# Kernel tuning notes

Measured on AMD Instinct MI355X. Metric: run time of the kernel, lower is better.

## Reference

```python
import jax, jax.numpy as jnp
import numpy as np

QNUM = 8
B, Q, K = 8, 32, 32
DIM = 2 ** QNUM  # v-circuit state dim; attn circuit uses 2*DIM (extra ancilla wire 0)

# --- 2x2 gate matrices (torchquantum conventions) ---

def ry_mat(theta):
    c = jnp.cos(theta / 2).astype(jnp.complex64)
    s = jnp.sin(theta / 2).astype(jnp.complex64)
    return jnp.stack([jnp.stack([c, -s], -1), jnp.stack([s, c], -1)], -2)

def rz_mat(theta):
    e = jnp.exp(-0.5j * theta)
    f = jnp.exp(0.5j * theta)
    z = jnp.zeros_like(e)
    return jnp.stack([jnp.stack([e, z], -1), jnp.stack([z, f], -1)], -2)

# --- state-vector gate application; wire 0 is the most-significant bit ---

def apply_1q(state, n, w, U):
    b = state.shape[0]
    st = state.reshape(b, 2 ** w, 2, 2 ** (n - w - 1))
    sub = 'bij,bajc->baic' if U.ndim == 3 else 'ij,bajc->baic'
    return jnp.einsum(sub, U, st).reshape(b, 2 ** n)

def apply_cnot(state, n, c, t):
    b = state.shape[0]
    st = state.reshape((b,) + (2,) * n)
    ca, ta = c + 1, t + 1
    c0 = jnp.take(st, 0, axis=ca)
    c1 = jnp.take(st, 1, axis=ca)
    c1 = jnp.flip(c1, axis=ta - 1 if ta > ca else ta)
    return jnp.stack([c0, c1], axis=ca).reshape(b, 2 ** n)

def apply_x(state, n, w):
    b = state.shape[0]
    st = state.reshape(b, 2 ** w, 2, -1)
    return jnp.flip(st, axis=2).reshape(b, 2 ** n)

def reset_wire(state, n, w):
    # torchquantum Reset: zero the |1> amplitude of the wire (no renorm)
    b = state.shape[0]
    st = state.reshape(b, 2 ** w, 2, -1)
    return st.at[:, :, 1, :].set(0).reshape(b, 2 ** n)

def init_state(b, n):
    return jnp.zeros((b, 2 ** n), jnp.complex64).at[:, 0].set(1)

# --- circuits ---

def v_circuit(value_flat, v_param):
    n = QNUM
    state = init_state(value_flat.shape[0], n)
    for i in range(n):  # v_embed: RY(value_i) on wire i (per-batch angle)
        state = apply_1q(state, n, i, ry_mat(value_flat[:, i]))
    for rep in range(6):  # inner_strent, repeat=6
        for i in range(n):  # fused RZ-RY-RZ (scalar params, shared over batch)
            U = rz_mat(v_param[rep, 2, i]) @ ry_mat(v_param[rep, 1, i]) @ rz_mat(v_param[rep, 0, i])
            state = apply_1q(state, n, i, U)
        for i in range(n):
            tg = (i + 1 + rep) % n
            if i == tg:
                tg = (tg + 1) % n
            state = apply_cnot(state, n, i, tg)
    return state

def attn_circuit(q_flat, k_flat, qk_param, attn_param):
    n = QNUM + 1  # wire 0 is the ancilla
    state = init_state(q_flat.shape[0], n)
    for i in range(QNUM):  # q_embed on wires 1..QNUM
        state = apply_1q(state, n, i + 1, ry_mat(q_flat[:, i]))
    for i in range(QNUM):  # RZ(qk[0,i]) then RY(qk[1,i]) fused
        state = apply_1q(state, n, i + 1, ry_mat(qk_param[1, i]) @ rz_mat(qk_param[0, i]))
    for i in range(QNUM):  # k_embed with -key
        state = apply_1q(state, n, i + 1, ry_mat(-k_flat[:, i]))
    state = apply_x(state, n, 0)
    for i in range(QNUM - 1):
        state = apply_1q(state, n, i + 1, ry_mat(attn_param[0, i]))
        state = apply_1q(state, n, i + 2, ry_mat(attn_param[1, i]))
        state = apply_cnot(state, n, i + 1, i + 2)
    state = apply_1q(state, n, QNUM, ry_mat(attn_param[0, QNUM - 1]))
    state = apply_1q(state, n, 0, ry_mat(attn_param[1, QNUM - 1]))
    state = apply_cnot(state, n, QNUM, 0)
    for w in range(1, QNUM + 1):
        state = reset_wire(state, n, w)
    return state

def forward(query, key, value, v_param, qk_param, attn_param):
    nb, nq, _ = query.shape
    nk = key.shape[1]
    # v circuit params/angles are independent of the query index, so simulate
    # over B*K and broadcast (identical math to the original B*Q*K repeat)
    v_states = v_circuit(value.reshape(nb * nk, QNUM), v_param).reshape(nb, nk, DIM)
    qf = jnp.broadcast_to(query[:, :, None, :], (nb, nq, nk, QNUM)).reshape(-1, QNUM)
    kf = jnp.broadcast_to(key[:, None, :, :], (nb, nq, nk, QNUM)).reshape(-1, QNUM)
    attn = attn_circuit(qf, kf, qk_param, attn_param).reshape(nb, nq, nk, 2, DIM)
    a0 = attn[:, :, :, 0, 0]  # amplitude of |00...0>
    a1 = attn[:, :, :, 1, 0]  # amplitude of |10...0> (ancilla=1)
    # sequential mixing v_new <- a0[k]*v_new + a1[k]*v_k, init e0; closed form:
    rev = jnp.flip(a0, axis=2)
    ecp = jnp.concatenate([jnp.ones_like(rev[:, :, :1]), jnp.cumprod(rev, axis=2)[:, :, :-1]], axis=2)
    suffix = jnp.flip(ecp, axis=2)  # suffix[j] = prod_{k>j} a0[k]
    total = jnp.prod(a0, axis=2)
    v_new = jnp.einsum('bqk,bkd->bqd', suffix * a1, v_states)
    v_new = v_new.at[:, :, 0].add(total)
    # StateEncoder normalization + MeasureAll(PauliZ)
    probs = v_new.real ** 2 + v_new.imag ** 2
    idx = jnp.arange(DIM)
    bits = (idx[None, :] >> (QNUM - 1 - jnp.arange(QNUM)[:, None])) & 1
    signs = (1 - 2 * bits).astype(jnp.float32)
    return jnp.einsum('bqd,wd->bqw', probs, signs) / jnp.sum(probs, -1, keepdims=True)

def setup_inputs():
    ks = jax.random.split(jax.random.key(0), 6)
    sigma = np.pi / 3
    return {
        'query': jax.random.normal(ks[0], (B, Q, QNUM), jnp.float32),
        'key': jax.random.normal(ks[1], (B, K, QNUM), jnp.float32),
        'value': jax.random.normal(ks[2], (B, K, QNUM), jnp.float32),
        'v_param': sigma * jax.random.normal(ks[3], (6, 3, QNUM), jnp.float32),
        'qk_param': sigma * jax.random.normal(ks[4], (3, QNUM), jnp.float32),
        'attn_param': sigma * jax.random.normal(ks[5], (2, QNUM), jnp.float32),
    }

def reference(query, key, value, v_param, qk_param, attn_param):
    return forward(query, key, value, v_param, qk_param, attn_param)
```

## Files before the change

### kernel.cpp

```cpp
#include <hip/hip_runtime.h>
#include <math.h>

#define NB 8
#define NQ 32
#define NK 32
#define DIM 256

struct c32 { float x, y; };
__device__ __forceinline__ c32 cmul(c32 a, c32 b) {
    return { a.x*b.x - a.y*b.y, a.x*b.y + a.y*b.x };
}

struct Maps { unsigned char m[6][8]; unsigned char r[6][8]; unsigned char fin[8]; };

constexpr unsigned gstep(int rep, unsigned y, int i) {
    int tgt = (i + 1 + rep) % 8;
    return y ^ (((y >> (7 - i)) & 1u) << (7 - tgt));
}
constexpr unsigned Lmap(int rep, unsigned x) {
    unsigned y = x;
    for (int i = 7; i >= 0; --i) y = gstep(rep, y, i);
    return y;
}
constexpr unsigned Linvmap(int rep, unsigned x) {
    unsigned y = x;
    for (int i = 0; i < 8; ++i) y = gstep(rep, y, i);
    return y;
}
constexpr Maps make_maps() {
    Maps mp{};
    unsigned Mc[8], Mic[8];
    for (int j2 = 0; j2 < 8; ++j2) { Mc[j2] = 1u << j2; Mic[j2] = 1u << j2; }
    for (int rep = 0; rep < 6; ++rep) {
        for (int bb = 0; bb < 8; ++bb) {
            mp.m[rep][bb] = (unsigned char)Mc[bb];
            unsigned row = 0;
            for (int k = 0; k < 8; ++k) row |= ((Mic[k] >> bb) & 1u) << k;
            mp.r[rep][bb] = (unsigned char)row;
        }
        unsigned nM[8], nMi[8];
        for (int j2 = 0; j2 < 8; ++j2) {
            unsigned v = Lmap(rep, 1u << j2), acc = 0;
            for (int k = 0; k < 8; ++k) if ((v >> k) & 1u) acc ^= Mc[k];
            nM[j2]  = acc;
            nMi[j2] = Linvmap(rep, Mic[j2]);
        }
        for (int j2 = 0; j2 < 8; ++j2) { Mc[j2] = nM[j2]; Mic[j2] = nMi[j2]; }
    }
    for (int j2 = 0; j2 < 8; ++j2) mp.fin[j2] = (unsigned char)Mic[j2];
    return mp;
}
constexpr Maps MAPS = make_maps();


__global__ __launch_bounds__(128) void k1_sim_coef(
        const float* __restrict__ query, const float* __restrict__ key,
        const float* __restrict__ value, const float* __restrict__ v_param,
        const float* __restrict__ qk_param, const float* __restrict__ attn_param,
        float2* __restrict__ vs, float2* __restrict__ coefg) {
    const int s  = blockIdx.x;
    const int b  = s >> 5;
    const int j  = s & 31;
    const int t  = threadIdx.x;
    const int ln = t & 63;

    if (t < 64) {
        __shared__ float2 U[48][4];
        if (ln < 48) {
            int rep = ln >> 3, w = ln & 7;
            float a   = v_param[(rep*3 + 0)*8 + w];
            float bb2 = v_param[(rep*3 + 1)*8 + w];
            float c   = v_param[(rep*3 + 2)*8 + w];
            float sb, cb;     __sincosf(bb2*0.5f, &sb, &cb);
            float sapc, capc; __sincosf((a + c)*0.5f, &sapc, &capc);
            float samc, camc; __sincosf((a - c)*0.5f, &samc, &camc);
            U[ln][0] = make_float2( cb*capc, -cb*sapc);
            U[ln][1] = make_float2(-sb*camc, -sb*samc);
            U[ln][2] = make_float2( sb*camc, -sb*samc);
            U[ln][3] = make_float2( cb*capc,  cb*sapc);
        }
        float cv[8], sv[8];
        #pragma unroll
        for (int i = 0; i < 8; ++i) __sincosf(value[s*8 + i]*0.5f, &sv[i], &cv[i]);
        float common = 1.f;
        #pragma unroll
        for (int i = 0; i < 6; ++i)
            common *= ((ln >> (5 - i)) & 1) ? sv[i] : cv[i];
        float2 amp[4];
        amp[0] = make_float2(common*cv[6]*cv[7], 0.f);
        amp[1] = make_float2(common*cv[6]*sv[7], 0.f);
        amp[2] = make_float2(common*sv[6]*cv[7], 0.f);
        amp[3] = make_float2(common*sv[6]*sv[7], 0.f);

        #pragma unroll
        for (int rep = 0; rep < 6; ++rep) {
            #pragma unroll
            for (int w = 0; w < 8; ++w) {
                const int g = rep*8 + w;
                const unsigned mm = MAPS.m[rep][7 - w];
                const unsigned rb = MAPS.r[rep][7 - w];
                const unsigned lm = mm >> 2;
                const unsigned sm = mm & 3;
                const float2 u00 = U[g][0], u01 = U[g][1];
                const float2 u10 = U[g][2], u11 = U[g][3];
                float2 P[4];
                if (sm == 0)      { P[0]=amp[0]; P[1]=amp[1]; P[2]=amp[2]; P[3]=amp[3]; }
                else if (sm == 1) { P[0]=amp[1]; P[1]=amp[0]; P[2]=amp[3]; P[3]=amp[2]; }
                else if (sm == 2) { P[0]=amp[2]; P[1]=amp[3]; P[2]=amp[0]; P[3]=amp[1]; }
                else              { P[0]=amp[3]; P[1]=amp[2]; P[2]=amp[1]; P[3]=amp[0]; }
                if (lm) {
                    #pragma unroll
                    for (int r2 = 0; r2 < 4; ++r2) {
                        P[r2].x = __shfl_xor(P[r2].x, (int)lm);
                        P[r2].y = __shfl_xor(P[r2].y, (int)lm);
                    }
                }
                const unsigned hx = __popc((unsigned)(ln << 2) & rb) & 1u;
                float2 na[4];
                #pragma unroll
                for (int r2 = 0; r2 < 4; ++r2) {
                    const bool h = (hx ^ (__popc((unsigned)r2 & rb) & 1u)) != 0u;
                    const float2 uo = h ? u11 : u00;
                    const float2 up = h ? u10 : u01;
                    na[r2].x = uo.x*amp[r2].x - uo.y*amp[r2].y + up.x*P[r2].x - up.y*P[r2].y;
                    na[r2].y = uo.x*amp[r2].y + uo.y*amp[r2].x + up.x*P[r2].y + up.y*P[r2].x;
                }
                #pragma unroll
                for (int r2 = 0; r2 < 4; ++r2) amp[r2] = na[r2];
            }
        }
        unsigned c0 = 0;
        #pragma unroll
        for (int kk = 0; kk < 6; ++kk)
            c0 ^= ((ln >> kk) & 1) ? (unsigned)MAPS.fin[kk + 2] : 0u;
        const int kst = j;
        float2* base = vs + ((size_t)(b*16 + (kst >> 1)) * 256) * 2 + (kst & 1);
        #pragma unroll
        for (int r2 = 0; r2 < 4; ++r2) {
            unsigned c = c0 ^ ((r2 & 1) ? (unsigned)MAPS.fin[0] : 0u)
                            ^ ((r2 & 2) ? (unsigned)MAPS.fin[1] : 0u);
            base[c*2] = amp[r2];
        }
    } else {
        const int k = ln >> 1, h = ln & 1;
        c32 f = { 1.f, 0.f };
        #pragma unroll
        for (int ii = 0; ii < 4; ++ii) {
            const int i = h*4 + ii;
            float qi  = query[(b*NQ + j)*8 + i];
            float ki  = key[(b*NK + k)*8 + i];
            float phi = attn_param[i] + ((i > 0) ? attn_param[8 + i - 1] : 0.f);
            float Th  = phi + qk_param[8 + i] - ki;
            float gam = qk_param[i] * 0.5f;
            c32 fi = {  __cosf(gam) * __cosf((Th + qi)*0.5f),
                       -__sinf(gam) * __cosf((Th - qi)*0.5f) };
            f = cmul(f, fi);
        }
        {
            c32 o2 = { __shfl_xor(f.x, 1), __shfl_xor(f.y, 1) };
            f = cmul(f, o2);
        }
        float fx = __shfl(f.x, 2*ln);
        float fy = __shfl(f.y, 2*ln);
        if (ln < 32) {
            const int kk = ln;
            float h7 = attn_param[15] * 0.5f;
            float s7 = __sinf(h7), c7 = __cosf(h7);
            c32 a0 = { -s7*fx, -s7*fy };
            c32 a1 = {  c7*fx,  c7*fy };
            c32 acc = a0;
            #pragma unroll
            for (int off = 1; off < 32; off <<= 1) {
                c32 v = { __shfl_down(acc.x, off), __shfl_down(acc.y, off) };
                if (kk + off < 32) acc = cmul(acc, v);
            }
            c32 S = { __shfl_down(acc.x, 1), __shfl_down(acc.y, 1) };
            if (kk == 31) { S.x = 1.f; S.y = 0.f; }
            c32 cf = cmul(S, a1);
            coefg[s*34 + kk] = make_float2(cf.x, cf.y);
            if (kk == 0) coefg[s*34 + 32] = make_float2(acc.x, acc.y);
        }
    }
}

__global__ __launch_bounds__(256) void k2_combine(
        const float2* __restrict__ vs, const float2* __restrict__ coefg,
        float* __restrict__ out) {
    const int bq = blockIdx.x;
    const int b = bq >> 5;
    const int q = bq & 31;
    const int t = threadIdx.x;

    __shared__ float2 coefL[33];
    __shared__ float prob[256];

    if (t < 33) coefL[t] = coefg[bq*34 + t];
    __syncthreads();

    {
        const float4* vb4 = reinterpret_cast<const float4*>(
            vs + ((size_t)b*16) * 512);
        c32 vn = { 0.f, 0.f };
        #pragma unroll
        for (int k2 = 0; k2 < 16; ++k2) {
            float4 v2 = vb4[k2*256 + t];
            float2 cfa = coefL[2*k2], cfb = coefL[2*k2 + 1];
            vn.x += cfa.x*v2.x - cfa.y*v2.y + cfb.x*v2.z - cfb.y*v2.w;
            vn.y += cfa.x*v2.y + cfa.y*v2.x + cfb.x*v2.w + cfb.y*v2.z;
        }
        if (t == 0) { vn.x += coefL[32].x; vn.y += coefL[32].y; }
        prob[t] = vn.x*vn.x + vn.y*vn.y;
    }
    __syncthreads();

    {
        const int gg = t >> 5, l = t & 31;
        float sp = 0.f, ss = 0.f;
        #pragma unroll
        for (int j2 = 0; j2 < 8; ++j2) {
            int d2 = l + 32*j2;
            float p = prob[d2];
            sp += p;
            ss += ((d2 >> (7 - gg)) & 1) ? -p : p;
        }
        #pragma unroll
        for (int off = 1; off < 32; off <<= 1) {
            sp += __shfl_xor(sp, off);
            ss += __shfl_xor(ss, off);
        }
        if (l == 0) out[(b*NQ + q)*8 + gg] = ss / sp;
    }
}

extern "C" void kernel_launch(void* const* d_in, const int* in_sizes, int n_in,
                              void* d_out, int out_size, void* d_ws, size_t ws_size,
                              hipStream_t stream) {
    const float* query      = (const float*)d_in[0];
    const float* key        = (const float*)d_in[1];
    const float* value      = (const float*)d_in[2];
    const float* v_param    = (const float*)d_in[3];
    const float* qk_param   = (const float*)d_in[4];
    const float* attn_param = (const float*)d_in[5];

    float2* vs    = (float2*)d_ws;
    float2* coefg = (float2*)((char*)d_ws + (size_t)512*1024);
    float*  out   = (float*)d_out;

    k1_sim_coef<<<NB*NK, 128, 0, stream>>>(query, key, value, v_param,
                                           qk_param, attn_param, vs, coefg);
    k2_combine<<<NB*NQ, 256, 0, stream>>>(vs, coefg, out);
}
```

Measured before the change: 18.53 us.

## Fuse simulation and combine kernels with per-batch atomic barrier

Merges the two kernels into one 256-thread launch. Coefficients stay in shared memory instead of going through global memory, and the dependency on v-states is enforced with a per-batch global atomic counter spin barrier. This removes a kernel launch boundary and the coefficient round-trip. In exchange it adds a hipMemsetAsync, relies on all 32 blocks of a batch being co-resident (256 blocks is fine on this GPU), and pays spin-wait overhead.

After: 34.89 us. 1.88x slower.

```diff
diff --git a/kernel.cpp b/kernel.cpp
--- a/kernel.cpp
+++ b/kernel.cpp
@@ -53,19 +53,24 @@
 constexpr Maps MAPS = make_maps();
 
 
-__global__ __launch_bounds__(128) void k1_sim_coef(
+__global__ __launch_bounds__(256) void fused_kernel(
         const float* __restrict__ query, const float* __restrict__ key,
         const float* __restrict__ value, const float* __restrict__ v_param,
         const float* __restrict__ qk_param, const float* __restrict__ attn_param,
-        float2* __restrict__ vs, float2* __restrict__ coefg) {
-    const int s  = blockIdx.x;
-    const int b  = s >> 5;
-    const int j  = s & 31;
-    const int t  = threadIdx.x;
-    const int ln = t & 63;
+        float2* __restrict__ vs, unsigned* __restrict__ ctr,
+        float* __restrict__ out) {
+    const int bid = blockIdx.x;
+    const int b   = bid & 7;
+    const int j   = bid >> 3;
+    const int s   = b * 32 + j;
+    const int t   = threadIdx.x;
+    const int ln  = t & 63;
+
+    __shared__ float2 U[48][4];
+    __shared__ float2 coefL[33];
+    __shared__ float prob[256];
 
     if (t < 64) {
-        __shared__ float2 U[48][4];
         if (ln < 48) {
             int rep = ln >> 3, w = ln & 7;
             float a   = v_param[(rep*3 + 0)*8 + w];
@@ -141,7 +146,7 @@
                             ^ ((r2 & 2) ? (unsigned)MAPS.fin[1] : 0u);
             base[c*2] = amp[r2];
         }
-    } else {
+    } else if (t < 128) {
         const int k = ln >> 1, h = ln & 1;
         c32 f = { 1.f, 0.f };
         #pragma unroll
@@ -177,24 +182,20 @@
             c32 S = { __shfl_down(acc.x, 1), __shfl_down(acc.y, 1) };
             if (kk == 31) { S.x = 1.f; S.y = 0.f; }
             c32 cf = cmul(S, a1);
-            coefg[s*34 + kk] = make_float2(cf.x, cf.y);
-            if (kk == 0) coefg[s*34 + 32] = make_float2(acc.x, acc.y);
-        }
-    }
-}
-
-__global__ __launch_bounds__(256) void k2_combine(
-        const float2* __restrict__ vs, const float2* __restrict__ coefg,
-        float* __restrict__ out) {
-    const int bq = blockIdx.x;
-    const int b = bq >> 5;
-    const int q = bq & 31;
-    const int t = threadIdx.x;
-
-    __shared__ float2 coefL[33];
-    __shared__ float prob[256];
-
-    if (t < 33) coefL[t] = coefg[bq*34 + t];
+            coefL[kk] = make_float2(cf.x, cf.y);
+            if (kk == 0) coefL[32] = make_float2(acc.x, acc.y);
+        }
+    }
+    __syncthreads();
+
+    if (t == 0) {
+        __threadfence();
+        __hip_atomic_fetch_add(&ctr[b*32], 1u, __ATOMIC_RELEASE,
+                               __HIP_MEMORY_SCOPE_AGENT);
+        while (__hip_atomic_load(&ctr[b*32], __ATOMIC_ACQUIRE,
+                                 __HIP_MEMORY_SCOPE_AGENT) < 32u)
+            __builtin_amdgcn_s_sleep(8);
+    }
     __syncthreads();
 
     {
@@ -228,7 +229,7 @@
             sp += __shfl_xor(sp, off);
             ss += __shfl_xor(ss, off);
         }
-        if (l == 0) out[(b*NQ + q)*8 + gg] = ss / sp;
+        if (l == 0) out[(b*NQ + j)*8 + gg] = ss / sp;
     }
 }
 
@@ -242,11 +243,11 @@
     const float* qk_param   = (const float*)d_in[4];
     const float* attn_param = (const float*)d_in[5];
 
-    float2* vs    = (float2*)d_ws;
-    float2* coefg = (float2*)((char*)d_ws + (size_t)512*1024);
-    float*  out   = (float*)d_out;
-
-    k1_sim_coef<<<NB*NK, 128, 0, stream>>>(query, key, value, v_param,
-                                           qk_param, attn_param, vs, coefg);
-    k2_combine<<<NB*NQ, 256, 0, stream>>>(vs, coefg, out);
-}
+    float2*   vs  = (float2*)d_ws;
+    unsigned* ctr = (unsigned*)((char*)d_ws + (size_t)512*1024);
+    float*    out = (float*)d_out;
+
+    hipMemsetAsync(ctr, 0, NB * 128, stream);
+    fused_kernel<<<NB*NK, 256, 0, stream>>>(query, key, value, v_param,
+                                            qk_param, attn_param, vs, ctr, out);
+}
```
